# Performance work log

Hardware: AMD Instinct MI355X
Metric: run time of the kernel (lower is better)

## Reference

```python
import jax, jax.numpy as jnp
import numpy as np

T, B = 8192, 4096  # n_time_steps, n_seqs


def setup_inputs() -> dict:
    key = jax.random.key(0)
    k1, k2 = jax.random.split(key)
    # Binary Bernoulli(0.5) observations, shape (T, B, 1), as the delta rule expects
    x = jnp.round(jax.random.uniform(k1, (T, B, 1), dtype=jnp.float32))
    # log-uniform learning rate per init_parameters: lr = 10 ** U(-2.5, -0.5)
    lr = 10.0 ** jax.random.uniform(k2, (), jnp.float32, minval=-2.5, maxval=-0.5)
    return {"x": x, "lr": lr}


def reference(x, lr):
    # DeltaRule forward, order=1 ('transition' / bigram) branch.
    # Gated EMA recurrence over time:
    #   p0_t = p0_{t-1} + lr * (x_t - p0_{t-1}) * (1 - x_{t-1})
    #   p1_t = p1_{t-1} + lr * (x_t - p1_{t-1}) * x_{t-1}
    # prediction_t = p0_t * (1 - x_t) + p1_t * x_t
    eff_lr = jnp.clip(lr, 0.0, 1.0)  # torch .clamp(0,1)
    obs = x[:, :, 0]  # (T, B)
    n_seqs = obs.shape[1]
    half = jnp.full((n_seqs,), 0.5, dtype=obs.dtype)
    init = (half, half, jnp.zeros((n_seqs,), dtype=obs.dtype))  # p0, p1, obs_prev

    def step(carry, x_t):
        p0, p1, obs_prev = carry
        p0 = p0 + eff_lr * (x_t - p0) * (1.0 - obs_prev)
        p1 = p1 + eff_lr * (x_t - p1) * obs_prev
        pred = p0 * (1.0 - x_t) + p1 * x_t
        return (p0, p1, x_t), pred

    _, preds = jax.lax.scan(step, init, obs)  # preds: (T, B)
    return preds[:, :, None]  # (T, B, 1), matching unsqueeze(2)
```

## Files before the change

kernel.cpp:

```cpp
#include <hip/hip_runtime.h>


constexpr int T_LEN  = 8192;
constexpr int B_SEQ  = 4096;
constexpr int B4     = B_SEQ / 4;
constexpr int CHUNK  = 64;
constexpr int NCHUNK = T_LEN / CHUNK;
constexpr int BLOCK  = 256;

__device__ __forceinline__ float clamp01(float v) {
    return fminf(fmaxf(v, 0.0f), 1.0f);
}

__global__ __launch_bounds__(BLOCK) void p1_compose(
    const float4* __restrict__ x4, const float* __restrict__ lr_ptr,
    float4* __restrict__ cA0, float4* __restrict__ cB0,
    float4* __restrict__ cA1, float4* __restrict__ cB1,
    uint4* __restrict__ bitsA, uint4* __restrict__ bitsB)
{
    const int i  = blockIdx.x * BLOCK + threadIdx.x;
    const int c  = blockIdx.y;
    const int t0 = c * CHUNK;
    const float lr = clamp01(*lr_ptr);

    float obs[4];
    if (c == 0) {
        obs[0]=obs[1]=obs[2]=obs[3]=0.f;
    } else {
        float4 o = x4[(size_t)(t0 - 1) * B4 + i];
        obs[0]=o.x; obs[1]=o.y; obs[2]=o.z; obs[3]=o.w;
    }

    float A0[4]  = {1.f,1.f,1.f,1.f}, Bc0[4] = {0.f,0.f,0.f,0.f};
    float A1[4]  = {1.f,1.f,1.f,1.f}, Bc1[4] = {0.f,0.f,0.f,0.f};
    unsigned long long bits[4] = {0ull,0ull,0ull,0ull};

    #pragma unroll 8
    for (int t = 0; t < CHUNK; ++t) {
        float4 xv = x4[(size_t)(t0 + t) * B4 + i];
        float xt[4] = {xv.x, xv.y, xv.z, xv.w};
        #pragma unroll
        for (int k = 0; k < 4; ++k) {
            bits[k] |= ((unsigned long long)(xt[k] != 0.0f)) << t;
            float g  = 1.0f - obs[k];
            float l0 = lr * g;
            float l1 = lr - l0;
            float a0 = 1.0f - l0;
            float a1 = 1.0f - l1;
            Bc0[k] = fmaf(a0, Bc0[k], l0 * xt[k]);  A0[k] *= a0;
            Bc1[k] = fmaf(a1, Bc1[k], l1 * xt[k]);  A1[k] *= a1;
            obs[k] = xt[k];
        }
    }

    const size_t idx = (size_t)c * B4 + i;
    cA0[idx] = make_float4(A0[0], A0[1], A0[2], A0[3]);
    cB0[idx] = make_float4(Bc0[0], Bc0[1], Bc0[2], Bc0[3]);
    cA1[idx] = make_float4(A1[0], A1[1], A1[2], A1[3]);
    cB1[idx] = make_float4(Bc1[0], Bc1[1], Bc1[2], Bc1[3]);
    bitsA[idx] = make_uint4((unsigned)bits[0], (unsigned)(bits[0] >> 32),
                            (unsigned)bits[1], (unsigned)(bits[1] >> 32));
    bitsB[idx] = make_uint4((unsigned)bits[2], (unsigned)(bits[2] >> 32),
                            (unsigned)bits[3], (unsigned)(bits[3] >> 32));
}


__device__ __forceinline__ float4 shfl_up4(float4 v, int d) {
    float4 r;
    r.x = __shfl_up(v.x, d);
    r.y = __shfl_up(v.y, d);
    r.z = __shfl_up(v.z, d);
    r.w = __shfl_up(v.w, d);
    return r;
}

#define COMPOSE4(Aa, Bb, pA, pB)                         \
    Bb.x = fmaf(Aa.x, pB.x, Bb.x);  Aa.x *= pA.x;        \
    Bb.y = fmaf(Aa.y, pB.y, Bb.y);  Aa.y *= pA.y;        \
    Bb.z = fmaf(Aa.z, pB.z, Bb.z);  Aa.z *= pA.z;        \
    Bb.w = fmaf(Aa.w, pB.w, Bb.w);  Aa.w *= pA.w;

__global__ __launch_bounds__(NCHUNK) void p2_scan(
    const float4* __restrict__ cA0, const float4* __restrict__ cB0,
    const float4* __restrict__ cA1, const float4* __restrict__ cB1,
    float4* __restrict__ sP0, float4* __restrict__ sP1)
{
    const int i    = blockIdx.x;
    const int c    = threadIdx.x;
    const int lane = c & 63;

    const size_t idx = (size_t)c * B4 + i;
    float4 A0 = cA0[idx], B0 = cB0[idx];
    float4 A1 = cA1[idx], B1 = cB1[idx];

    #pragma unroll
    for (int d = 1; d < 64; d <<= 1) {
        float4 pA0 = shfl_up4(A0, d), pB0 = shfl_up4(B0, d);
        float4 pA1 = shfl_up4(A1, d), pB1 = shfl_up4(B1, d);
        if (lane >= d) {
            COMPOSE4(A0, B0, pA0, pB0);
            COMPOSE4(A1, B1, pA1, pB1);
        }
    }

    __shared__ float4 tA0, tB0, tA1, tB1;
    __shared__ float4 sA0[NCHUNK], sB0[NCHUNK], sA1[NCHUNK], sB1[NCHUNK];

    if (c == 63) { tA0 = A0; tB0 = B0; tA1 = A1; tB1 = B1; }
    __syncthreads();
    if (c >= 64) {
        COMPOSE4(A0, B0, tA0, tB0);
        COMPOSE4(A1, B1, tA1, tB1);
    }
    sA0[c] = A0; sB0[c] = B0; sA1[c] = A1; sB1[c] = B1;
    __syncthreads();

    float4 eA0, eB0, eA1, eB1;
    if (c == 0) {
        eA0 = make_float4(1,1,1,1); eB0 = make_float4(0,0,0,0);
        eA1 = make_float4(1,1,1,1); eB1 = make_float4(0,0,0,0);
    } else {
        eA0 = sA0[c-1]; eB0 = sB0[c-1];
        eA1 = sA1[c-1]; eB1 = sB1[c-1];
    }
    sP0[idx] = make_float4(fmaf(eA0.x, 0.5f, eB0.x), fmaf(eA0.y, 0.5f, eB0.y),
                           fmaf(eA0.z, 0.5f, eB0.z), fmaf(eA0.w, 0.5f, eB0.w));
    sP1[idx] = make_float4(fmaf(eA1.x, 0.5f, eB1.x), fmaf(eA1.y, 0.5f, eB1.y),
                           fmaf(eA1.z, 0.5f, eB1.z), fmaf(eA1.w, 0.5f, eB1.w));
}

__global__ __launch_bounds__(BLOCK) void p3_emit(
    const float4* __restrict__ x4, const float* __restrict__ lr_ptr,
    const float4* __restrict__ sP0, const float4* __restrict__ sP1,
    const uint4* __restrict__ bitsA, const uint4* __restrict__ bitsB,
    float4* __restrict__ out4)
{
    const int i  = blockIdx.x * BLOCK + threadIdx.x;
    const int c  = blockIdx.y;
    const int t0 = c * CHUNK;
    const float lr = clamp01(*lr_ptr);

    const size_t idx = (size_t)c * B4 + i;
    float4 P0 = sP0[idx], P1 = sP1[idx];
    float p0[4] = {P0.x, P0.y, P0.z, P0.w};
    float p1[4] = {P1.x, P1.y, P1.z, P1.w};

    uint4 ba = bitsA[idx], bb = bitsB[idx];
    unsigned lo[4] = {ba.x, ba.z, bb.x, bb.z};
    unsigned hi[4] = {ba.y, ba.w, bb.y, bb.w};

    float obs[4];
    if (c == 0) {
        obs[0]=obs[1]=obs[2]=obs[3]=0.f;
    } else {
        float4 o = x4[(size_t)(t0 - 1) * B4 + i];
        obs[0]=o.x; obs[1]=o.y; obs[2]=o.z; obs[3]=o.w;
    }

    #pragma unroll 8
    for (int t = 0; t < CHUNK; ++t) {
        float pr[4];
        #pragma unroll
        for (int k = 0; k < 4; ++k) {
            unsigned w   = (t < 32) ? lo[k] : hi[k];
            unsigned bit = (w >> (t & 31)) & 1u;
            float xf = (float)bit;
            float g  = 1.0f - obs[k];
            float l0 = lr * g;
            float l1 = lr - l0;
            p0[k] = fmaf(l0, xf - p0[k], p0[k]);
            p1[k] = fmaf(l1, xf - p1[k], p1[k]);
            pr[k] = bit ? p1[k] : p0[k];
            obs[k] = xf;
        }
        out4[(size_t)(t0 + t) * B4 + i] = make_float4(pr[0], pr[1], pr[2], pr[3]);
    }
}

extern "C" void kernel_launch(void* const* d_in, const int* in_sizes, int n_in,
                              void* d_out, int out_size, void* d_ws, size_t ws_size,
                              hipStream_t stream) {
    const float4* x4  = (const float4*)d_in[0];
    const float*  lr  = (const float*)d_in[1];
    float4*       out = (float4*)d_out;

    const size_t n = (size_t)NCHUNK * B4;
    float4* cA0 = (float4*)d_ws;
    float4* cB0 = cA0 + n;
    float4* cA1 = cB0 + n;
    float4* cB1 = cA1 + n;
    float4* sP0 = cB1 + n;
    float4* sP1 = sP0 + n;
    uint4*  bitsA = (uint4*)(sP1 + n);
    uint4*  bitsB = bitsA + n;

    dim3 grid13(B4 / BLOCK, NCHUNK);
    p1_compose<<<grid13, BLOCK, 0, stream>>>(x4, lr, cA0, cB0, cA1, cB1, bitsA, bitsB);
    p2_scan<<<dim3(B4), NCHUNK, 0, stream>>>(cA0, cB0, cA1, cB1, sP0, sP1);
    p3_emit<<<grid13, BLOCK, 0, stream>>>(x4, lr, sP0, sP1, bitsA, bitsB, out);
}
```

Measured before the change: 252.0 us.

## Halve chunk length, interleave chunk maps, and generalize cross-wave scan

Cuts the time chunk from 64 to 32 steps, doubling the number of chunks. The chunk-scan kernel now runs 256 threads (4 waves) per block and combines wave totals through shared memory in a serial loop. The per-chunk affine maps (A0, B0, A1, B1) are packed into one interleaved buffer, as are the two start-state arrays. Observation bits now fit in one 32-bit word per lane, which removes the lo/hi word select in the emit loop. The aim is more parallelism in phases 1 and 3 and less indexing work, at the cost of a larger intermediate workspace and more scan traffic.

```diff
diff --git a/kernel.cpp b/kernel.cpp
--- a/kernel.cpp
+++ b/kernel.cpp
@@ -4,9 +4,10 @@
 constexpr int T_LEN  = 8192;
 constexpr int B_SEQ  = 4096;
 constexpr int B4     = B_SEQ / 4;
-constexpr int CHUNK  = 64;
+constexpr int CHUNK  = 32;
 constexpr int NCHUNK = T_LEN / CHUNK;
 constexpr int BLOCK  = 256;
+constexpr int NWAVE  = NCHUNK / 64;
 
 __device__ __forceinline__ float clamp01(float v) {
     return fminf(fmaxf(v, 0.0f), 1.0f);
@@ -14,9 +15,7 @@
 
 __global__ __launch_bounds__(BLOCK) void p1_compose(
     const float4* __restrict__ x4, const float* __restrict__ lr_ptr,
-    float4* __restrict__ cA0, float4* __restrict__ cB0,
-    float4* __restrict__ cA1, float4* __restrict__ cB1,
-    uint4* __restrict__ bitsA, uint4* __restrict__ bitsB)
+    float4* __restrict__ maps, uint4* __restrict__ bitsOut)
 {
     const int i  = blockIdx.x * BLOCK + threadIdx.x;
     const int c  = blockIdx.y;
@@ -33,7 +32,7 @@
 
     float A0[4]  = {1.f,1.f,1.f,1.f}, Bc0[4] = {0.f,0.f,0.f,0.f};
     float A1[4]  = {1.f,1.f,1.f,1.f}, Bc1[4] = {0.f,0.f,0.f,0.f};
-    unsigned long long bits[4] = {0ull,0ull,0ull,0ull};
+    unsigned bits[4] = {0u,0u,0u,0u};
 
     #pragma unroll 8
     for (int t = 0; t < CHUNK; ++t) {
@@ -41,7 +40,7 @@
         float xt[4] = {xv.x, xv.y, xv.z, xv.w};
         #pragma unroll
         for (int k = 0; k < 4; ++k) {
-            bits[k] |= ((unsigned long long)(xt[k] != 0.0f)) << t;
+            bits[k] |= ((unsigned)(xt[k] != 0.0f)) << t;
             float g  = 1.0f - obs[k];
             float l0 = lr * g;
             float l1 = lr - l0;
@@ -53,15 +52,12 @@
         }
     }
 
-    const size_t idx = (size_t)c * B4 + i;
-    cA0[idx] = make_float4(A0[0], A0[1], A0[2], A0[3]);
-    cB0[idx] = make_float4(Bc0[0], Bc0[1], Bc0[2], Bc0[3]);
-    cA1[idx] = make_float4(A1[0], A1[1], A1[2], A1[3]);
-    cB1[idx] = make_float4(Bc1[0], Bc1[1], Bc1[2], Bc1[3]);
-    bitsA[idx] = make_uint4((unsigned)bits[0], (unsigned)(bits[0] >> 32),
-                            (unsigned)bits[1], (unsigned)(bits[1] >> 32));
-    bitsB[idx] = make_uint4((unsigned)bits[2], (unsigned)(bits[2] >> 32),
-                            (unsigned)bits[3], (unsigned)(bits[3] >> 32));
+    const size_t base = ((size_t)c * B4 + i) * 4;
+    maps[base + 0] = make_float4(A0[0],  A0[1],  A0[2],  A0[3]);
+    maps[base + 1] = make_float4(Bc0[0], Bc0[1], Bc0[2], Bc0[3]);
+    maps[base + 2] = make_float4(A1[0],  A1[1],  A1[2],  A1[3]);
+    maps[base + 3] = make_float4(Bc1[0], Bc1[1], Bc1[2], Bc1[3]);
+    bitsOut[(size_t)c * B4 + i] = make_uint4(bits[0], bits[1], bits[2], bits[3]);
 }
 
 
@@ -81,17 +77,16 @@
     Bb.w = fmaf(Aa.w, pB.w, Bb.w);  Aa.w *= pA.w;
 
 __global__ __launch_bounds__(NCHUNK) void p2_scan(
-    const float4* __restrict__ cA0, const float4* __restrict__ cB0,
-    const float4* __restrict__ cA1, const float4* __restrict__ cB1,
-    float4* __restrict__ sP0, float4* __restrict__ sP1)
+    const float4* __restrict__ maps, float4* __restrict__ sP)
 {
     const int i    = blockIdx.x;
     const int c    = threadIdx.x;
     const int lane = c & 63;
+    const int wv   = c >> 6;
 
-    const size_t idx = (size_t)c * B4 + i;
-    float4 A0 = cA0[idx], B0 = cB0[idx];
-    float4 A1 = cA1[idx], B1 = cB1[idx];
+    const size_t base = ((size_t)c * B4 + i) * 4;
+    float4 A0 = maps[base + 0], B0 = maps[base + 1];
+    float4 A1 = maps[base + 2], B1 = maps[base + 3];
 
     #pragma unroll
     for (int d = 1; d < 64; d <<= 1) {
@@ -103,15 +98,15 @@
         }
     }
 
-    __shared__ float4 tA0, tB0, tA1, tB1;
+    __shared__ float4 wA0[NWAVE], wB0[NWAVE], wA1[NWAVE], wB1[NWAVE];
+    if (lane == 63) { wA0[wv] = A0; wB0[wv] = B0; wA1[wv] = A1; wB1[wv] = B1; }
+    __syncthreads();
+    for (int w = wv - 1; w >= 0; --w) {
+        COMPOSE4(A0, B0, wA0[w], wB0[w]);
+        COMPOSE4(A1, B1, wA1[w], wB1[w]);
+    }
+
     __shared__ float4 sA0[NCHUNK], sB0[NCHUNK], sA1[NCHUNK], sB1[NCHUNK];
-
-    if (c == 63) { tA0 = A0; tB0 = B0; tA1 = A1; tB1 = B1; }
-    __syncthreads();
-    if (c >= 64) {
-        COMPOSE4(A0, B0, tA0, tB0);
-        COMPOSE4(A1, B1, tA1, tB1);
-    }
     sA0[c] = A0; sB0[c] = B0; sA1[c] = A1; sB1[c] = B1;
     __syncthreads();
 
@@ -123,16 +118,16 @@
         eA0 = sA0[c-1]; eB0 = sB0[c-1];
         eA1 = sA1[c-1]; eB1 = sB1[c-1];
     }
-    sP0[idx] = make_float4(fmaf(eA0.x, 0.5f, eB0.x), fmaf(eA0.y, 0.5f, eB0.y),
-                           fmaf(eA0.z, 0.5f, eB0.z), fmaf(eA0.w, 0.5f, eB0.w));
-    sP1[idx] = make_float4(fmaf(eA1.x, 0.5f, eB1.x), fmaf(eA1.y, 0.5f, eB1.y),
-                           fmaf(eA1.z, 0.5f, eB1.z), fmaf(eA1.w, 0.5f, eB1.w));
+    const size_t idx = (size_t)c * B4 + i;
+    sP[idx*2 + 0] = make_float4(fmaf(eA0.x, 0.5f, eB0.x), fmaf(eA0.y, 0.5f, eB0.y),
+                                fmaf(eA0.z, 0.5f, eB0.z), fmaf(eA0.w, 0.5f, eB0.w));
+    sP[idx*2 + 1] = make_float4(fmaf(eA1.x, 0.5f, eB1.x), fmaf(eA1.y, 0.5f, eB1.y),
+                                fmaf(eA1.z, 0.5f, eB1.z), fmaf(eA1.w, 0.5f, eB1.w));
 }
 
 __global__ __launch_bounds__(BLOCK) void p3_emit(
     const float4* __restrict__ x4, const float* __restrict__ lr_ptr,
-    const float4* __restrict__ sP0, const float4* __restrict__ sP1,
-    const uint4* __restrict__ bitsA, const uint4* __restrict__ bitsB,
+    const float4* __restrict__ sP, const uint4* __restrict__ bitsIn,
     float4* __restrict__ out4)
 {
     const int i  = blockIdx.x * BLOCK + threadIdx.x;
@@ -141,13 +136,12 @@
     const float lr = clamp01(*lr_ptr);
 
     const size_t idx = (size_t)c * B4 + i;
-    float4 P0 = sP0[idx], P1 = sP1[idx];
+    float4 P0 = sP[idx*2 + 0], P1 = sP[idx*2 + 1];
     float p0[4] = {P0.x, P0.y, P0.z, P0.w};
     float p1[4] = {P1.x, P1.y, P1.z, P1.w};
 
-    uint4 ba = bitsA[idx], bb = bitsB[idx];
-    unsigned lo[4] = {ba.x, ba.z, bb.x, bb.z};
-    unsigned hi[4] = {ba.y, ba.w, bb.y, bb.w};
+    uint4 bv = bitsIn[idx];
+    unsigned w[4] = {bv.x, bv.y, bv.z, bv.w};
 
     float obs[4];
     if (c == 0) {
@@ -162,8 +156,7 @@
         float pr[4];
         #pragma unroll
         for (int k = 0; k < 4; ++k) {
-            unsigned w   = (t < 32) ? lo[k] : hi[k];
-            unsigned bit = (w >> (t & 31)) & 1u;
+            unsigned bit = (w[k] >> t) & 1u;
             float xf = (float)bit;
             float g  = 1.0f - obs[k];
             float l0 = lr * g;
@@ -185,17 +178,12 @@
     float4*       out = (float4*)d_out;
 
     const size_t n = (size_t)NCHUNK * B4;
-    float4* cA0 = (float4*)d_ws;
-    float4* cB0 = cA0 + n;
-    float4* cA1 = cB0 + n;
-    float4* cB1 = cA1 + n;
-    float4* sP0 = cB1 + n;
-    float4* sP1 = sP0 + n;
-    uint4*  bitsA = (uint4*)(sP1 + n);
-    uint4*  bitsB = bitsA + n;
+    float4* maps = (float4*)d_ws;
+    float4* sP   = maps + 4 * n;
+    uint4*  bits = (uint4*)(sP + 2 * n);
 
     dim3 grid13(B4 / BLOCK, NCHUNK);
-    p1_compose<<<grid13, BLOCK, 0, stream>>>(x4, lr, cA0, cB0, cA1, cB1, bitsA, bitsB);
-    p2_scan<<<dim3(B4), NCHUNK, 0, stream>>>(cA0, cB0, cA1, cB1, sP0, sP1);
-    p3_emit<<<grid13, BLOCK, 0, stream>>>(x4, lr, sP0, sP1, bitsA, bitsB, out);
+    p1_compose<<<grid13, BLOCK, 0, stream>>>(x4, lr, maps, bits);
+    p2_scan<<<dim3(B4), NCHUNK, 0, stream>>>(maps, sP);
+    p3_emit<<<grid13, BLOCK, 0, stream>>>(x4, lr, sP, bits, out);
 }
```

Result: no change. 253.6 us (+0.6%).
